# Kernel tuning notes

Measured on AMD Instinct MI355X. Metric: run time of the kernel, lower is better.

The kernel has to match this reference:

```python
import jax, jax.numpy as jnp
import numpy as np

HEADS = 16  # module init arg `heads`


def setup_inputs() -> dict:
    key = jax.random.key(0)
    k1, k2, k3 = jax.random.split(key, 3)
    B, T, D = 2, 2048, 1024
    x = jax.random.normal(k1, (B, T, D), dtype=jnp.float32)
    w_qkv = jax.random.normal(k2, (D, 3 * D), dtype=jnp.float32) * (1.0 / np.sqrt(D))
    w_proj = jax.random.normal(k3, (D, D), dtype=jnp.float32) * (1.0 / np.sqrt(D))
    b_proj = jnp.zeros((D,), dtype=jnp.float32)
    return {"x": x, "w_qkv": w_qkv, "w_proj": w_proj, "b_proj": b_proj,
            "window": 16, "stride": 16}


def reference(x, w_qkv, w_proj, b_proj, window, stride):
    B, T, D = x.shape
    H = HEADS
    hd = D // H
    scale = 1.0 / np.sqrt(hd)

    qkv = x @ w_qkv                              # [B,T,3D]
    qkv = qkv.reshape(B, T, 3, H, hd)
    q = jnp.transpose(qkv[:, :, 0], (0, 2, 1, 3))  # [B,H,T,hd]
    k = jnp.transpose(qkv[:, :, 1], (0, 2, 1, 3))
    v = jnp.transpose(qkv[:, :, 2], (0, 2, 1, 3))

    # Local window attention: pad front with zeros (matches F.pad), gather
    # sliding windows so patches[..., t, w, :] = k_padded[..., t + w, :].
    pad = window - 1
    k_pad = jnp.pad(k, ((0, 0), (0, 0), (pad, 0), (0, 0)))
    v_pad = jnp.pad(v, ((0, 0), (0, 0), (pad, 0), (0, 0)))
    win_idx = jnp.arange(T)[:, None] + jnp.arange(window)[None, :]  # [T,W]
    pk = k_pad[:, :, win_idx]                    # [B,H,T,W,hd]
    pv = v_pad[:, :, win_idx]                    # [B,H,T,W,hd]

    attn_local = jnp.einsum('bhtd,bhtwd->bhtw', q, pk) * scale
    attn_local = jax.nn.softmax(attn_local, axis=-1)  # zero-pad keys included, as in torch
    out_local = jnp.einsum('bhtw,bhtwd->bhtd', attn_local, pv)

    # Strided global attention
    g_idx = jnp.arange(0, T, stride)
    kg = k[:, :, g_idx]                          # [B,H,G,hd]
    vg = v[:, :, g_idx]
    attn_g = jnp.einsum('bhtd,bhgd->bhtg', q, kg) * scale
    attn_g = jax.nn.softmax(attn_g, axis=-1)
    out_global = jnp.einsum('bhtg,bhgd->bhtd', attn_g, vg)

    out = out_local + out_global                 # [B,H,T,hd]
    out = jnp.transpose(out, (0, 2, 1, 3)).reshape(B, T, D)
    return out @ w_proj + b_proj
```

## Files before the change

### kernel.cpp

```cpp
#include <hip/hip_runtime.h>
#include <hip/hip_bf16.h>

#define BB 2
#define TT 2048
#define DD 1024
#define HH 16
#define HD 64
#define WIN 16
#define NG 128
#define QKVLD 3072

typedef __bf16 bf16x8 __attribute__((ext_vector_type(8)));
typedef _Float16 f16x8 __attribute__((ext_vector_type(8)));
typedef float f32x4 __attribute__((ext_vector_type(4)));
typedef _Float16 h2 __attribute__((ext_vector_type(2)));
typedef __fp16 pk2_t __attribute__((ext_vector_type(2)));

__device__ __forceinline__ unsigned short f2bf(float f) {
    union { float f; unsigned int i; } x; x.f = f;
    unsigned int r = x.i + 0x7FFFu + ((x.i >> 16) & 1u);
    return (unsigned short)(r >> 16);
}
__device__ __forceinline__ unsigned short f2h(float f) {
    union { _Float16 h; unsigned short u; } x; x.h = (_Float16)f; return x.u;
}
__device__ __forceinline__ unsigned int pk2h(float lo, float hi) {
    union { pk2_t h; unsigned int u; } X;
    X.h = __builtin_amdgcn_cvt_pkrtz(lo, hi);
    return X.u;
}

__device__ __forceinline__ void gll16(const unsigned short* g, unsigned short* l) {
    __builtin_amdgcn_global_load_lds(
        (const __attribute__((address_space(1))) void*)g,
        (__attribute__((address_space(3))) void*)l,
        16, 0, 0);
}

__global__ __launch_bounds__(256) void prepass_kernel(
    const float* __restrict__ x,
    const float* __restrict__ w_qkv,
    const float* __restrict__ w_proj,
    unsigned short* __restrict__ xb,
    unsigned short* __restrict__ wqkvT,
    unsigned short* __restrict__ wprojT)
{
    __shared__ float tile[64][65];
    const int bid = blockIdx.x;
    const int tid = threadIdx.x;

    if (bid < 2048) {
        const size_t i = ((size_t)bid * 256 + tid) * 8;
        float4 f0 = *(const float4*)(x + i);
        float4 f1 = *(const float4*)(x + i + 4);
        ushort4 a = { f2bf(f0.x), f2bf(f0.y), f2bf(f0.z), f2bf(f0.w) };
        ushort4 b = { f2bf(f1.x), f2bf(f1.y), f2bf(f1.z), f2bf(f1.w) };
        *(ushort4*)(xb + i) = a;
        *(ushort4*)(xb + i + 4) = b;
        return;
    }

    const float* w;
    unsigned short* wT;
    int nblk, kblk, N;
    if (bid < 2816) {
        const int b2 = bid - 2048;
        w = w_qkv; wT = wqkvT; N = 3072;
        nblk = b2 % 48; kblk = b2 / 48;
    } else {
        const int b2 = bid - 2816;
        w = w_proj; wT = wprojT; N = 1024;
        nblk = b2 % 16; kblk = b2 / 16;
    }
    const int K = 1024;
    const int n0 = nblk * 64, k0 = kblk * 64;

    {
        const int krow = tid >> 2;
        const int nc0  = (tid & 3) * 16;
        const float* src = w + (size_t)(k0 + krow) * N + n0 + nc0;
        float4 f0 = *(const float4*)(src);
        float4 f1 = *(const float4*)(src + 4);
        float4 f2 = *(const float4*)(src + 8);
        float4 f3 = *(const float4*)(src + 12);
        *(float4*)&tile[krow][nc0]      = f0;
        *(float4*)&tile[krow][nc0 + 4]  = f1;
        *(float4*)&tile[krow][nc0 + 8]  = f2;
        *(float4*)&tile[krow][nc0 + 12] = f3;
    }
    __syncthreads();
    #pragma unroll
    for (int rep = 0; rep < 2; ++rep) {
        const int n   = (tid >> 3) + rep * 32;
        const int kc0 = (tid & 7) * 8;
        union { uint4 v; unsigned short u[8]; } o;
        #pragma unroll
        for (int j = 0; j < 8; ++j) o.u[j] = f2bf(tile[kc0 + j][n]);
        *(uint4*)(wT + (size_t)(n0 + n) * K + k0 + kc0) = o.v;
    }
}

template<int MODE, int TN>
__global__ __launch_bounds__(256) void gemm_kernel(
    const unsigned short* __restrict__ A,
    const unsigned short* __restrict__ Bt,
    void* __restrict__ Cp,
    const float* __restrict__ bias,
    int M, int N, int K)
{
    constexpr int NJ = TN / 32;
    constexpr int BR = TN / 4;
    __shared__ __align__(16) unsigned short As[128 * 32];
    __shared__ __align__(16) unsigned short Bs[TN * 32];
    const int tid  = threadIdx.x;
    const int wave = tid >> 6;
    const int lane = tid & 63;
    const int lm   = lane & 15;
    const int quad = lane >> 4;
    const int wm   = (wave >> 1) * 64;
    const int wn   = (wave & 1) * (TN / 2);
    const int bm   = blockIdx.y * 128;
    const int bn   = blockIdx.x * TN;

    f32x4 acc[4][NJ];
    const f32x4 z4 = { 0.f, 0.f, 0.f, 0.f };
    #pragma unroll
    for (int i = 0; i < 4; ++i)
        #pragma unroll
        for (int j = 0; j < NJ; ++j) acc[i][j] = z4;

    const int lrow = lane >> 2, lcol = (lane & 3) * 8;
    const unsigned short* gA0 = A  + (size_t)(bm + wave * 32 + lrow) * K + lcol;
    const unsigned short* gA1 = gA0 + (size_t)16 * K;
    const unsigned short* gB0 = Bt + (size_t)(bn + wave * BR + lrow) * K + lcol;
    const unsigned short* gB1 = gB0 + (size_t)16 * K;
    unsigned short* lA0 = &As[(wave * 32) * 32];
    unsigned short* lA1 = &As[(wave * 32 + 16) * 32];
    unsigned short* lB0 = &Bs[(wave * BR) * 32];
    unsigned short* lB1 = &Bs[(wave * BR + 16) * 32];

    for (int k0 = 0; k0 < K; k0 += 32) {
        __syncthreads();
        gll16(gA0 + k0, lA0);
        gll16(gA1 + k0, lA1);
        gll16(gB0 + k0, lB0);
        if constexpr (BR == 32) gll16(gB1 + k0, lB1);
        __syncthreads();
        bf16x8 af[4], bfr[NJ];
        #pragma unroll
        for (int i = 0; i < 4; ++i)
            af[i] = *(const bf16x8*)&As[(wm + i * 16 + lm) * 32 + quad * 8];
        #pragma unroll
        for (int j = 0; j < NJ; ++j)
            bfr[j] = *(const bf16x8*)&Bs[(wn + j * 16 + lm) * 32 + quad * 8];
        #pragma unroll
        for (int i = 0; i < 4; ++i)
            #pragma unroll
            for (int j = 0; j < NJ; ++j)
                acc[i][j] = __builtin_amdgcn_mfma_f32_16x16x32_bf16(
                    af[i], bfr[j], acc[i][j], 0, 0, 0);
    }

    #pragma unroll
    for (int i = 0; i < 4; ++i) {
        #pragma unroll
        for (int r = 0; r < 4; ++r) {
            const int row = bm + wm + i * 16 + quad * 4 + r;
            #pragma unroll
            for (int j = 0; j < NJ; ++j) {
                const int col = bn + wn + j * 16 + lm;
                float v = acc[i][j][r];
                if constexpr (MODE == 0) {
                    ((unsigned short*)Cp)[(size_t)row * N + col] = f2h(v);
                } else {
                    ((float*)Cp)[(size_t)row * N + col] = v + bias[col];
                }
            }
        }
    }
}

__device__ __forceinline__ f16x8 pfrag(unsigned int fa0, unsigned int fa1,
                                       unsigned int fb0, unsigned int fb1,
                                       int quad) {
    const unsigned int t16_0 = (quad == 2) ? fb0 : fa0;
    const unsigned int t16_1 = (quad == 2) ? fb1 : fa1;
    const unsigned int t32_0 = (quad == 0) ? fb0 : fa0;
    const unsigned int t32_1 = (quad == 0) ? fb1 : fa1;
    const unsigned int t48_0 = (quad == 1) ? fb0 : fa0;
    const unsigned int t48_1 = (quad == 1) ? fb1 : fa1;
    const unsigned int s16_0 = (unsigned int)__shfl_xor((int)t16_0, 16, 64);
    const unsigned int s16_1 = (unsigned int)__shfl_xor((int)t16_1, 16, 64);
    const unsigned int s32_0 = (unsigned int)__shfl_xor((int)t32_0, 32, 64);
    const unsigned int s32_1 = (unsigned int)__shfl_xor((int)t32_1, 32, 64);
    const unsigned int s48_0 = (unsigned int)__shfl_xor((int)t48_0, 48, 64);
    const unsigned int s48_1 = (unsigned int)__shfl_xor((int)t48_1, 48, 64);
    unsigned int w0, w1, w2, w3;
    if (quad == 0)      { w0 = fa0;   w1 = fa1;   w2 = s16_0; w3 = s16_1; }
    else if (quad == 1) { w0 = s48_0; w1 = s48_1; w2 = s32_0; w3 = s32_1; }
    else if (quad == 2) { w0 = s32_0; w1 = s32_1; w2 = s48_0; w3 = s48_1; }
    else                { w0 = s16_0; w1 = s16_1; w2 = fb0;   w3 = fb1;   }
    union { unsigned int u[4]; f16x8 v; } R;
    R.u[0] = w0; R.u[1] = w1; R.u[2] = w2; R.u[3] = w3;
    return R.v;
}

__global__ __launch_bounds__(256, 4) void attn_kernel(
    const unsigned short* __restrict__ qkv,
    unsigned short* __restrict__ attn_out)
{
    __shared__ __align__(16) unsigned short smem[14976];
    unsigned short* const Kg  = smem;
    unsigned short* const Kl  = smem + 9216;
    unsigned short* const VgT = smem;
    unsigned short* const VlT = smem + 8704;
    unsigned short* const Ep  = smem + 9216;

    const int tid  = threadIdx.x;
    const int wave = tid >> 6;
    const int lane = tid & 63;
    const int lm   = lane & 15;
    const int quad = lane >> 4;
    const int bx   = blockIdx.x;
    const int bh   = bx >> 5;
    const int t0   = (bx & 31) * 64;
    const int b    = bh >> 4;
    const int h    = bh & 15;

    const size_t baseQ = (size_t)(b * TT) * QKVLD + h * HD;

    const int r  = tid >> 1;
    const int hf = tid & 1;
    uint4 vg[4], vl[4];
    {
        const unsigned short* ks = qkv + baseQ + 1024 + (size_t)(16 * r) * QKVLD + hf * 32;
        const unsigned short* vs = ks + 1024;
        unsigned short* kd = Kg + r * 72 + hf * 32;
        #pragma unroll
        for (int j = 0; j < 4; ++j) *(uint4*)(kd + j * 8) = *(const uint4*)(ks + j * 8);
        #pragma unroll
        for (int j = 0; j < 4; ++j) vg[j] = *(const uint4*)(vs + j * 8);

        if (r < 80) {
            const int tl = t0 - 15 + r;
            unsigned short* kld = Kl + r * 72 + hf * 32;
            if (tl < 0 || tl >= TT) {
                const uint4 z = { 0, 0, 0, 0 };
                #pragma unroll
                for (int j = 0; j < 4; ++j) { *(uint4*)(kld + j * 8) = z; vl[j] = z; }
            } else {
                const unsigned short* kls = qkv + baseQ + 1024 + (size_t)tl * QKVLD + hf * 32;
                const unsigned short* vls = kls + 1024;
                #pragma unroll
                for (int j = 0; j < 4; ++j) *(uint4*)(kld + j * 8) = *(const uint4*)(kls + j * 8);
                #pragma unroll
                for (int j = 0; j < 4; ++j) vl[j] = *(const uint4*)(vls + j * 8);
            }
        }
    }

    f16x8 qf[2];
    {
        const unsigned short* qrow = qkv + baseQ + (size_t)(t0 + 16 * wave + lm) * QKVLD;
        const h2 sc = { (_Float16)0.125f, (_Float16)0.125f };
        #pragma unroll
        for (int c = 0; c < 2; ++c) {
            union { uint4 u; h2 hh[4]; f16x8 v; } U;
            U.u = *(const uint4*)(qrow + c * 32 + quad * 8);
            #pragma unroll
            for (int k = 0; k < 4; ++k) U.hh[k] *= sc;
            qf[c] = U.v;
        }
    }

    __syncthreads();

    f32x4 sg[8], sl[2];
    const f32x4 z4 = { 0.f, 0.f, 0.f, 0.f };
    #pragma unroll
    for (int f = 0; f < 8; ++f) sg[f] = z4;
    sl[0] = z4; sl[1] = z4;
    #pragma unroll
    for (int f = 0; f < 8; ++f)
        #pragma unroll
        for (int c = 0; c < 2; ++c)
            sg[f] = __builtin_amdgcn_mfma_f32_16x16x32_f16(
                *(const f16x8*)&Kg[(16 * f + lm) * 72 + c * 32 + quad * 8], qf[c],
                sg[f], 0, 0, 0);
    #pragma unroll
    for (int f = 0; f < 2; ++f)
        #pragma unroll
        for (int c = 0; c < 2; ++c)
            sl[f] = __builtin_amdgcn_mfma_f32_16x16x32_f16(
                *(const f16x8*)&Kl[(16 * wave + 16 * f + lm) * 72 + c * 32 + quad * 8], qf[c],
                sl[f], 0, 0, 0);

    float invg, invl;
    {
        float dg = 0.f, dl = 0.f;
        #pragma unroll
        for (int f = 0; f < 8; ++f)
            #pragma unroll
            for (int rr = 0; rr < 4; ++rr) {
                float e = __expf(sg[f][rr]); sg[f][rr] = e; dg += e;
            }
        #pragma unroll
        for (int f = 0; f < 2; ++f)
            #pragma unroll
            for (int rr = 0; rr < 4; ++rr) {
                const int j2 = 16 * f + quad * 4 + rr;
                const bool in = (j2 >= lm) && (j2 <= lm + 15);
                float e = in ? __expf(sl[f][rr]) : 0.f;
                sl[f][rr] = e; dl += e;
            }
        dg += __shfl_xor(dg, 16, 64);
        dg += __shfl_xor(dg, 32, 64);
        dl += __shfl_xor(dl, 16, 64);
        dl += __shfl_xor(dl, 32, 64);
        invg = 1.f / dg;
        invl = 1.f / dl;
    }

    f16x8 pa0, pa1, pa2, pa3, pal;
    {
        #pragma unroll
        for (int f = 0; f < 8; ++f)
            #pragma unroll
            for (int rr = 0; rr < 4; ++rr) sg[f][rr] *= invg;
        #pragma unroll
        for (int f = 0; f < 2; ++f)
            #pragma unroll
            for (int rr = 0; rr < 4; ++rr) sl[f][rr] *= invl;
        pa0 = pfrag(pk2h(sg[0][0], sg[0][1]), pk2h(sg[0][2], sg[0][3]),
                    pk2h(sg[1][0], sg[1][1]), pk2h(sg[1][2], sg[1][3]), quad);
        pa1 = pfrag(pk2h(sg[2][0], sg[2][1]), pk2h(sg[2][2], sg[2][3]),
                    pk2h(sg[3][0], sg[3][1]), pk2h(sg[3][2], sg[3][3]), quad);
        pa2 = pfrag(pk2h(sg[4][0], sg[4][1]), pk2h(sg[4][2], sg[4][3]),
                    pk2h(sg[5][0], sg[5][1]), pk2h(sg[5][2], sg[5][3]), quad);
        pa3 = pfrag(pk2h(sg[6][0], sg[6][1]), pk2h(sg[6][2], sg[6][3]),
                    pk2h(sg[7][0], sg[7][1]), pk2h(sg[7][2], sg[7][3]), quad);
        pal = pfrag(pk2h(sl[0][0], sl[0][1]), pk2h(sl[0][2], sl[0][3]),
                    pk2h(sl[1][0], sl[1][1]), pk2h(sl[1][2], sl[1][3]), quad);
    }

    __syncthreads();

    {
        union { uint4 u[4]; unsigned short s[32]; } Ug;
        #pragma unroll
        for (int j = 0; j < 4; ++j) Ug.u[j] = vg[j];
        #pragma unroll
        for (int j = 0; j < 32; ++j) VgT[(hf * 32 + j) * 136 + r] = Ug.s[j];
        if (r < 80) {
            union { uint4 u[4]; unsigned short s[32]; } Ul;
            #pragma unroll
            for (int j = 0; j < 4; ++j) Ul.u[j] = vl[j];
            #pragma unroll
            for (int j = 0; j < 32; ++j) VlT[(hf * 32 + j) * 88 + r] = Ul.s[j];
        }
    }

    __syncthreads();

    f32x4 o[4];
    #pragma unroll
    for (int c = 0; c < 4; ++c) o[c] = z4;
    #pragma unroll
    for (int c = 0; c < 4; ++c) {
        o[c] = __builtin_amdgcn_mfma_f32_16x16x32_f16(
            pa0, *(const f16x8*)&VgT[(16 * c + lm) * 136 + 0 * 32 + quad * 8], o[c], 0, 0, 0);
        o[c] = __builtin_amdgcn_mfma_f32_16x16x32_f16(
            pa1, *(const f16x8*)&VgT[(16 * c + lm) * 136 + 1 * 32 + quad * 8], o[c], 0, 0, 0);
        o[c] = __builtin_amdgcn_mfma_f32_16x16x32_f16(
            pa2, *(const f16x8*)&VgT[(16 * c + lm) * 136 + 2 * 32 + quad * 8], o[c], 0, 0, 0);
        o[c] = __builtin_amdgcn_mfma_f32_16x16x32_f16(
            pa3, *(const f16x8*)&VgT[(16 * c + lm) * 136 + 3 * 32 + quad * 8], o[c], 0, 0, 0);
        o[c] = __builtin_amdgcn_mfma_f32_16x16x32_f16(
            pal, *(const f16x8*)&VlT[(16 * c + lm) * 88 + 16 * wave + quad * 8], o[c], 0, 0, 0);
    }

    __syncthreads();

    {
        unsigned short* const Pw = Ep + wave * (16 * 72);
        #pragma unroll
        for (int rr = 0; rr < 4; ++rr) {
            unsigned short* orow_p = Pw + (quad * 4 + rr) * 72;
            #pragma unroll
            for (int c = 0; c < 4; ++c) orow_p[16 * c + lm] = f2bf(o[c][rr]);
        }
        const int orow = lane >> 2;
        const int ocol = (lane & 3) * 16;
        const uint4 d0 = *(const uint4*)&Pw[orow * 72 + ocol];
        const uint4 d1 = *(const uint4*)&Pw[orow * 72 + ocol + 8];
        unsigned short* dst = attn_out + (size_t)(b * TT + t0 + 16 * wave + orow) * DD + h * HD + ocol;
        *(uint4*)(dst)     = d0;
        *(uint4*)(dst + 8) = d1;
    }
}

extern "C" void kernel_launch(void* const* d_in, const int* in_sizes, int n_in,
                              void* d_out, int out_size, void* d_ws, size_t ws_size,
                              hipStream_t stream) {
    const float* x      = (const float*)d_in[0];
    const float* w_qkv  = (const float*)d_in[1];
    const float* w_proj = (const float*)d_in[2];
    const float* b_proj = (const float*)d_in[3];

    char* ws = (char*)d_ws;
    unsigned short* qkv    = (unsigned short*)ws;
    unsigned short* xb     = (unsigned short*)(ws + 25165824);
    unsigned short* attnb  = xb;
    unsigned short* wqkvT  = (unsigned short*)(ws + 25165824 + 8388608);
    unsigned short* wprojT = (unsigned short*)(ws + 25165824 + 8388608 + 6291456);
    float* out = (float*)d_out;

    prepass_kernel<<<3072, 256, 0, stream>>>(x, w_qkv, w_proj, xb, wqkvT, wprojT);

    gemm_kernel<0, 128><<<dim3(3072 / 128, 4096 / 128), 256, 0, stream>>>(
        xb, wqkvT, qkv, nullptr, 4096, 3072, 1024);

    attn_kernel<<<dim3(BB * HH * (TT / 64)), 256, 0, stream>>>(qkv, attnb);

    gemm_kernel<1, 64><<<dim3(1024 / 64, 4096 / 128), 256, 0, stream>>>(
        attnb, wprojT, out, b_proj, 4096, 1024, 1024);
}
```

Before: 157.3 us.

## Stage GEMM epilogue through LDS, remap blocks per XCD, add MFMA priority hints

The GEMM epilogue now writes accumulators into a per-wave LDS staging buffer and then stores 16-byte vectors to global memory, replacing scattered 2/4-byte stores. Block indices are remapped so that blocks landing on the same XCD work on contiguous column tiles, which is meant to improve L2 reuse. The attention kernel wraps its MFMA sections in s_setprio to favour matrix issue. The extra 36KB of LDS per GEMM block may reduce occupancy, and the remap assumes gridDim.x is divisible by 8.

```diff
diff --git a/kernel.cpp b/kernel.cpp
--- a/kernel.cpp
+++ b/kernel.cpp
@@ -112,6 +112,7 @@
     constexpr int BR = TN / 4;
     __shared__ __align__(16) unsigned short As[128 * 32];
     __shared__ __align__(16) unsigned short Bs[TN * 32];
+    __shared__ __align__(16) unsigned char epi[4 * 9216];
     const int tid  = threadIdx.x;
     const int wave = tid >> 6;
     const int lane = tid & 63;
@@ -119,8 +120,16 @@
     const int quad = lane >> 4;
     const int wm   = (wave >> 1) * 64;
     const int wn   = (wave & 1) * (TN / 2);
-    const int bm   = blockIdx.y * 128;
-    const int bn   = blockIdx.x * TN;
+
+    const int flat = blockIdx.y * gridDim.x + blockIdx.x;
+    const int cpx  = gridDim.x >> 3;
+    const int xcd  = flat & 7;
+    const int idx  = flat >> 3;
+    const int qy   = idx / gridDim.y;
+    const int bxs  = xcd * cpx + qy;
+    const int bys  = idx - qy * gridDim.y;
+    const int bm   = bys * 128;
+    const int bn   = bxs * TN;
 
     f32x4 acc[4][NJ];
     const f32x4 z4 = { 0.f, 0.f, 0.f, 0.f };
@@ -161,20 +170,37 @@
                     af[i], bfr[j], acc[i][j], 0, 0, 0);
     }
 
-    #pragma unroll
-    for (int i = 0; i < 4; ++i) {
-        #pragma unroll
-        for (int r = 0; r < 4; ++r) {
-            const int row = bm + wm + i * 16 + quad * 4 + r;
-            #pragma unroll
-            for (int j = 0; j < NJ; ++j) {
-                const int col = bn + wn + j * 16 + lm;
-                float v = acc[i][j][r];
-                if constexpr (MODE == 0) {
-                    ((unsigned short*)Cp)[(size_t)row * N + col] = f2h(v);
-                } else {
-                    ((float*)Cp)[(size_t)row * N + col] = v + bias[col];
+    {
+        unsigned short* ep16 = (unsigned short*)&epi[wave * 9216];
+        float*          ep32 = (float*)&epi[wave * 9216];
+        #pragma unroll
+        for (int i = 0; i < 4; ++i) {
+            #pragma unroll
+            for (int r = 0; r < 4; ++r) {
+                const int erow = i * 16 + quad * 4 + r;
+                #pragma unroll
+                for (int j = 0; j < NJ; ++j) {
+                    const float v = acc[i][j][r];
+                    if constexpr (MODE == 0) {
+                        ep16[erow * 72 + j * 16 + lm] = f2h(v);
+                    } else {
+                        ep32[erow * 36 + j * 16 + lm] = v + bias[bn + wn + j * 16 + lm];
+                    }
                 }
+            }
+        }
+        const int prow = lane >> 3;
+        const int pcol = (lane & 7) * 16;
+        #pragma unroll
+        for (int p = 0; p < 8; ++p) {
+            const int row = p * 8 + prow;
+            const uint4 d = *(const uint4*)(&epi[wave * 9216] + row * 144 + pcol);
+            if constexpr (MODE == 0) {
+                *(uint4*)((unsigned short*)Cp + (size_t)(bm + wm + row) * N
+                          + bn + wn + (lane & 7) * 8) = d;
+            } else {
+                *(uint4*)((float*)Cp + (size_t)(bm + wm + row) * N
+                          + bn + wn + (lane & 7) * 4) = d;
             }
         }
     }
@@ -280,6 +306,7 @@
     #pragma unroll
     for (int f = 0; f < 8; ++f) sg[f] = z4;
     sl[0] = z4; sl[1] = z4;
+    __builtin_amdgcn_s_setprio(1);
     #pragma unroll
     for (int f = 0; f < 8; ++f)
         #pragma unroll
@@ -294,6 +321,7 @@
             sl[f] = __builtin_amdgcn_mfma_f32_16x16x32_f16(
                 *(const f16x8*)&Kl[(16 * wave + 16 * f + lm) * 72 + c * 32 + quad * 8], qf[c],
                 sl[f], 0, 0, 0);
+    __builtin_amdgcn_s_setprio(0);
 
     float invg, invl;
     {
@@ -365,6 +393,7 @@
     f32x4 o[4];
     #pragma unroll
     for (int c = 0; c < 4; ++c) o[c] = z4;
+    __builtin_amdgcn_s_setprio(1);
     #pragma unroll
     for (int c = 0; c < 4; ++c) {
         o[c] = __builtin_amdgcn_mfma_f32_16x16x32_f16(
@@ -378,6 +407,7 @@
         o[c] = __builtin_amdgcn_mfma_f32_16x16x32_f16(
             pal, *(const f16x8*)&VlT[(16 * c + lm) * 88 + 16 * wave + quad * 8], o[c], 0, 0, 0);
     }
+    __builtin_amdgcn_s_setprio(0);
 
     __syncthreads();
 
```

Result: no change. 159.8 us (+1.6%).
